# Optimization experiments

Hardware: AMD Instinct MI355X
Metric: run time of the kernel (lower is better)

Reference implementation:

```python
import jax, jax.numpy as jnp
import numpy as np

I4_CLIP = 7.0
NUM_HEADS = 16
NUM_KV_HEADS = 4
HEAD_DIM = 64
ROPE_BASE = 10000.0


def fake_quant_i4(w):
    # per-row int4 symmetric fake quantization with straight-through estimator
    row_max = jnp.maximum(jnp.max(jnp.abs(w), axis=-1, keepdims=True), 1e-8)
    scale = row_max / I4_CLIP
    w_deq = jnp.clip(jnp.round(w / scale), -I4_CLIP, I4_CLIP) * scale
    return w + jax.lax.stop_gradient(w_deq - w)


def rms_norm(x):
    eps = jnp.asarray(jnp.finfo(x.dtype).eps, x.dtype)
    return x * jax.lax.rsqrt(jnp.mean(x * x, axis=-1, keepdims=True) + eps)


def rope_cos_sin(seqlen, dtype):
    inv_freq = 1.0 / (ROPE_BASE ** (jnp.arange(0, HEAD_DIM, 2, dtype=jnp.float32) / HEAD_DIM))
    freqs = jnp.outer(jnp.arange(seqlen, dtype=jnp.float32), inv_freq)  # [S, hd/2]
    return jnp.cos(freqs).astype(dtype), jnp.sin(freqs).astype(dtype)


def apply_rotary(x, cos, sin):
    # x: [B, H, S, hd]; cos/sin: [S, hd/2] broadcast over B, H
    half = x.shape[-1] // 2
    x1, x2 = x[..., :half], x[..., half:]
    return jnp.concatenate((x1 * cos + x2 * sin, -x1 * sin + x2 * cos), axis=-1)


def setup_inputs() -> dict:
    key = jax.random.key(0)
    ks = jax.random.split(key, 6)
    dim = NUM_HEADS * HEAD_DIM
    kv_dim = NUM_KV_HEADS * HEAD_DIM
    return {
        "x": jax.random.normal(ks[0], (2, 2048, dim), jnp.float32),
        "w_q": jax.random.normal(ks[1], (dim, dim), jnp.float32) * 0.02,
        "w_k": jax.random.normal(ks[2], (kv_dim, dim), jnp.float32) * 0.02,
        "w_v": jax.random.normal(ks[3], (kv_dim, dim), jnp.float32) * 0.02,
        "w_proj": jax.random.normal(ks[4], (dim, dim), jnp.float32) * 0.02,
        "q_gain": jnp.ones((NUM_HEADS,), jnp.float32),
    }


def reference(x, w_q, w_k, w_v, w_proj, q_gain):
    bsz, seqlen, dim = x.shape
    rep = NUM_HEADS // NUM_KV_HEADS

    wq, wk, wv, wp = (fake_quant_i4(w) for w in (w_q, w_k, w_v, w_proj))

    # projections: F.linear(x, W) = x @ W.T -> [B, S, out]; split heads -> [B, H, S, hd]
    q = (x @ wq.T).reshape(bsz, seqlen, NUM_HEADS, HEAD_DIM).transpose(0, 2, 1, 3)
    k = (x @ wk.T).reshape(bsz, seqlen, NUM_KV_HEADS, HEAD_DIM).transpose(0, 2, 1, 3)
    v = (x @ wv.T).reshape(bsz, seqlen, NUM_KV_HEADS, HEAD_DIM).transpose(0, 2, 1, 3)

    q, k = rms_norm(q), rms_norm(k)
    cos, sin = rope_cos_sin(seqlen, q.dtype)
    q = apply_rotary(q, cos, sin)
    k = apply_rotary(k, cos, sin)
    q = q * q_gain.astype(q.dtype)[None, :, None, None]

    # GQA: expand kv heads
    k = jnp.repeat(k, rep, axis=1)
    v = jnp.repeat(v, rep, axis=1)

    # causal SDPA
    scale = 1.0 / np.sqrt(HEAD_DIM)
    scores = jnp.einsum("bhqd,bhkd->bhqk", q, k) * scale
    causal = jnp.tril(jnp.ones((seqlen, seqlen), dtype=bool))
    scores = jnp.where(causal, scores, jnp.asarray(-jnp.inf, scores.dtype))
    attn = jax.nn.softmax(scores, axis=-1)
    y = jnp.einsum("bhqk,bhkd->bhqd", attn, v)

    y = y.transpose(0, 2, 1, 3).reshape(bsz, seqlen, dim)
    return y @ wp.T
```

## Files before the change

### kernel.cpp

```cpp
#include <hip/hip_runtime.h>


typedef __bf16 bf16x8 __attribute__((ext_vector_type(8)));
typedef __bf16 bf16x4 __attribute__((ext_vector_type(4)));
typedef float  f32x4  __attribute__((ext_vector_type(4)));

__device__ __forceinline__ unsigned short f2bf(float f) {
  __bf16 h = (__bf16)f;
  return __builtin_bit_cast(unsigned short, h);
}

__global__ void quant_all(const float* __restrict__ wq, const float* __restrict__ wk,
                          const float* __restrict__ wv, const float* __restrict__ wp,
                          unsigned short* __restrict__ wqkv,
                          unsigned short* __restrict__ wpb) {
  int row = blockIdx.x;
  const float* s;
  unsigned short* d;
  if (row < 1024)      { s = wq + (size_t)row * 1024;          d = wqkv + (size_t)row * 1024; }
  else if (row < 1280) { s = wk + (size_t)(row - 1024) * 1024; d = wqkv + (size_t)row * 1024; }
  else if (row < 1536) { s = wv + (size_t)(row - 1280) * 1024; d = wqkv + (size_t)row * 1024; }
  else                 { s = wp + (size_t)(row - 1536) * 1024; d = wpb + (size_t)(row - 1536) * 1024; }
  int t = threadIdx.x;
  float v[4]; float mx = 0.f;
#pragma unroll
  for (int i = 0; i < 4; i++) { v[i] = s[t + 256 * i]; mx = fmaxf(mx, fabsf(v[i])); }
#pragma unroll
  for (int m = 1; m < 64; m <<= 1) mx = fmaxf(mx, __shfl_xor(mx, m));
  __shared__ float smx[4];
  if ((t & 63) == 0) smx[t >> 6] = mx;
  __syncthreads();
  mx = fmaxf(fmaxf(smx[0], smx[1]), fmaxf(smx[2], smx[3]));
  mx = fmaxf(mx, 1e-8f);
  float scale = mx / 7.0f;
#pragma unroll
  for (int i = 0; i < 4; i++) {
    float q = rintf(v[i] / scale);
    q = fminf(fmaxf(q, -7.0f), 7.0f);
    d[t + 256 * i] = f2bf(q * scale);
  }
}

__global__ void cvt_bf16(const float* __restrict__ src,
                         unsigned short* __restrict__ dst, int n) {
  int i = (blockIdx.x * 256 + threadIdx.x) * 4;
  if (i >= n) return;
  float4 f = *(const float4*)(src + i);
  ushort4 o;
  o.x = f2bf(f.x); o.y = f2bf(f.y); o.z = f2bf(f.z); o.w = f2bf(f.w);
  *(ushort4*)(dst + i) = o;
}

#define GLDS(g, l)                                                            \
  __builtin_amdgcn_global_load_lds((const __attribute__((address_space(1))) void*)(g), \
                                   (__attribute__((address_space(3))) void*)(l), 16, 0, 0)

__global__ __launch_bounds__(256, 2) void gemm_bt(
    const unsigned short* __restrict__ A, const unsigned short* __restrict__ Bw,
    float* __restrict__ C, int N, int K, int nbn) {
  int bm = blockIdx.x / nbn, bn = blockIdx.x % nbn;
  int tid = threadIdx.x, w = tid >> 6, lane = tid & 63;
  int l15 = lane & 15, lh = lane >> 4;
  __shared__ __align__(16) unsigned short ldsA[2][128 * 64];
  __shared__ __align__(16) unsigned short ldsB[2][128 * 64];
  int wr = w >> 1, wc = w & 1;
  f32x4 zero = {0.f, 0.f, 0.f, 0.f};
  f32x4 acc[4][4];
#pragma unroll
  for (int i = 0; i < 4; i++)
#pragma unroll
    for (int j = 0; j < 4; j++) acc[i][j] = zero;

  int srow = lane >> 3, schunk = (lane & 7) ^ (lane >> 3);
  const unsigned short* gA0 = A  + (size_t)(bm * 128 + srow) * K + schunk * 8;
  const unsigned short* gB0 = Bw + (size_t)(bn * 128 + srow) * K + schunk * 8;

  int nk = K >> 6;
#pragma unroll
  for (int it = 0; it < 4; it++) {
    int seg = w * 4 + it;
    GLDS(gA0 + (size_t)(seg * 8) * K, (unsigned short*)ldsA[0] + seg * 512);
    GLDS(gB0 + (size_t)(seg * 8) * K, (unsigned short*)ldsB[0] + seg * 512);
  }
  __syncthreads();
  int cur = 0;
  for (int kt = 0; kt < nk; kt++) {
    if (kt + 1 < nk) {
      int k0 = (kt + 1) * 64;
#pragma unroll
      for (int it = 0; it < 4; it++) {
        int seg = w * 4 + it;
        GLDS(gA0 + (size_t)(seg * 8) * K + k0, (unsigned short*)ldsA[cur ^ 1] + seg * 512);
        GLDS(gB0 + (size_t)(seg * 8) * K + k0, (unsigned short*)ldsB[cur ^ 1] + seg * 512);
      }
    }
    const unsigned short* cA = ldsA[cur];
    const unsigned short* cB = ldsB[cur];
#pragma unroll
    for (int ks = 0; ks < 2; ks++) {
      bf16x8 af[4], bfr[4];
#pragma unroll
      for (int fm = 0; fm < 4; fm++) {
        int row = wr * 64 + fm * 16 + l15;
        int slot = (ks * 4 + lh) ^ (row & 7);
        af[fm] = *(const bf16x8*)(cA + row * 64 + slot * 8);
      }
#pragma unroll
      for (int fn = 0; fn < 4; fn++) {
        int row = wc * 64 + fn * 16 + l15;
        int slot = (ks * 4 + lh) ^ (row & 7);
        bfr[fn] = *(const bf16x8*)(cB + row * 64 + slot * 8);
      }
#pragma unroll
      for (int fm = 0; fm < 4; fm++)
#pragma unroll
        for (int fn = 0; fn < 4; fn++)
          acc[fm][fn] = __builtin_amdgcn_mfma_f32_16x16x32_bf16(af[fm], bfr[fn], acc[fm][fn], 0, 0, 0);
    }
    __syncthreads();
    cur ^= 1;
  }
#pragma unroll
  for (int fm = 0; fm < 4; fm++) {
    int r0 = bm * 128 + wr * 64 + fm * 16 + lh * 4;
#pragma unroll
    for (int fn = 0; fn < 4; fn++) {
      int c = bn * 128 + wc * 64 + fn * 16 + l15;
#pragma unroll
      for (int reg = 0; reg < 4; reg++)
        C[(size_t)(r0 + reg) * N + c] = acc[fm][fn][reg];
    }
  }
}

__global__ __launch_bounds__(256, 2) void gemm_qkv(
    const unsigned short* __restrict__ A, const unsigned short* __restrict__ Bw,
    const float* __restrict__ gainp,
    unsigned short* __restrict__ qb, unsigned short* __restrict__ kbp,
    unsigned short* __restrict__ vbp) {
  const int K = 1024;
  int bm = blockIdx.x / 12, bn = blockIdx.x % 12;
  int tid = threadIdx.x, w = tid >> 6, lane = tid & 63;
  int l15 = lane & 15, lh = lane >> 4;
  __shared__ __align__(16) unsigned short ldsA[2][128 * 64];
  __shared__ __align__(16) unsigned short ldsB[2][128 * 64];
  int wr = w >> 1, wc = w & 1;
  f32x4 zero = {0.f, 0.f, 0.f, 0.f};
  f32x4 acc[4][4];
#pragma unroll
  for (int i = 0; i < 4; i++)
#pragma unroll
    for (int j = 0; j < 4; j++) acc[i][j] = zero;

  int srow = lane >> 3, schunk = (lane & 7) ^ (lane >> 3);
  const unsigned short* gA0 = A  + (size_t)(bm * 128 + srow) * K + schunk * 8;
  const unsigned short* gB0 = Bw + (size_t)(bn * 128 + srow) * K + schunk * 8;

#pragma unroll
  for (int it = 0; it < 4; it++) {
    int seg = w * 4 + it;
    GLDS(gA0 + (size_t)(seg * 8) * K, (unsigned short*)ldsA[0] + seg * 512);
    GLDS(gB0 + (size_t)(seg * 8) * K, (unsigned short*)ldsB[0] + seg * 512);
  }
  __syncthreads();
  int cur = 0;
  for (int kt = 0; kt < 16; kt++) {
    if (kt + 1 < 16) {
      int k0 = (kt + 1) * 64;
#pragma unroll
      for (int it = 0; it < 4; it++) {
        int seg = w * 4 + it;
        GLDS(gA0 + (size_t)(seg * 8) * K + k0, (unsigned short*)ldsA[cur ^ 1] + seg * 512);
        GLDS(gB0 + (size_t)(seg * 8) * K + k0, (unsigned short*)ldsB[cur ^ 1] + seg * 512);
      }
    }
    const unsigned short* cA = ldsA[cur];
    const unsigned short* cB = ldsB[cur];
#pragma unroll
    for (int ks = 0; ks < 2; ks++) {
      bf16x8 af[4], bfr[4];
#pragma unroll
      for (int fm = 0; fm < 4; fm++) {
        int row = wr * 64 + fm * 16 + l15;
        int slot = (ks * 4 + lh) ^ (row & 7);
        af[fm] = *(const bf16x8*)(cA + row * 64 + slot * 8);
      }
#pragma unroll
      for (int fn = 0; fn < 4; fn++) {
        int row = wc * 64 + fn * 16 + l15;
        int slot = (ks * 4 + lh) ^ (row & 7);
        bfr[fn] = *(const bf16x8*)(cB + row * 64 + slot * 8);
      }
#pragma unroll
      for (int fm = 0; fm < 4; fm++)
#pragma unroll
        for (int fn = 0; fn < 4; fn++)
          acc[fm][fn] = __builtin_amdgcn_mfma_f32_16x16x32_bf16(af[fm], bfr[fn], acc[fm][fn], 0, 0, 0);
    }
    __syncthreads();
    cur ^= 1;
  }

  int hid = bn * 2 + wc;
  int rbase = bm * 128 + wr * 64;
  if (hid >= 20) {
    int vh = hid - 20;
#pragma unroll
    for (int fm = 0; fm < 4; fm++)
#pragma unroll
      for (int reg = 0; reg < 4; reg++) {
        int r = rbase + fm * 16 + lh * 4 + reg;
        int b = r >> 11, s = r & 2047;
        unsigned short* dst = vbp + (((size_t)(b * 4 + vh) * 2048 + s) << 6);
#pragma unroll
        for (int fn = 0; fn < 4; fn++)
          dst[fn * 16 + l15] = f2bf(acc[fm][fn][reg]);
      }
  } else {
    bool isq = hid < 16;
    float gn = isq ? gainp[hid] : 1.0f;
    float invf0 = __expf(-0.28782313662425572f * (float)l15);
    float invf1 = __expf(-0.28782313662425572f * (float)(l15 + 16));
#pragma unroll
    for (int fm = 0; fm < 4; fm++)
#pragma unroll
      for (int reg = 0; reg < 4; reg++) {
        float y0 = acc[fm][0][reg], y1 = acc[fm][1][reg];
        float y2 = acc[fm][2][reg], y3 = acc[fm][3][reg];
        float ss = y0 * y0 + y1 * y1 + y2 * y2 + y3 * y3;
        ss += __shfl_xor(ss, 1); ss += __shfl_xor(ss, 2);
        ss += __shfl_xor(ss, 4); ss += __shfl_xor(ss, 8);
        float rn = rsqrtf(ss * 0.015625f + 1.1920929e-7f);
        y0 *= rn; y1 *= rn; y2 *= rn; y3 *= rn;
        int r = rbase + fm * 16 + lh * 4 + reg;
        int b = r >> 11, s = r & 2047;
        float c0, s0n, c1, s1n;
        __sincosf((float)s * invf0, &s0n, &c0);
        __sincosf((float)s * invf1, &s1n, &c1);
        float o0 = (y0 * c0 + y2 * s0n) * gn;
        float o1 = (y1 * c1 + y3 * s1n) * gn;
        float o2 = (y2 * c0 - y0 * s0n) * gn;
        float o3 = (y3 * c1 - y1 * s1n) * gn;
        unsigned short* dst = isq
          ? qb  + (((size_t)(b * 16 + hid) * 2048 + s) << 6)
          : kbp + (((size_t)(b * 4 + (hid - 16)) * 2048 + s) << 6);
        dst[l15]      = f2bf(o0);
        dst[l15 + 16] = f2bf(o1);
        dst[l15 + 32] = f2bf(o2);
        dst[l15 + 48] = f2bf(o3);
      }
  }
}

__global__ void v_transpose(const unsigned short* __restrict__ vbp,
                            unsigned short* __restrict__ vt) {
  int bid = blockIdx.x;
  int st = bid & 31, bk = bid >> 5;
  __shared__ unsigned short tile[64][72];
  int t = threadIdx.x;
  int sl = t >> 2, d0 = (t & 3) * 16;
  const unsigned short* src = vbp + (((size_t)bk * 2048 + st * 64 + sl) << 6) + d0;
  *(ushort4*)&tile[sl][d0]      = *(const ushort4*)(src);
  *(ushort4*)&tile[sl][d0 + 4]  = *(const ushort4*)(src + 4);
  *(ushort4*)&tile[sl][d0 + 8]  = *(const ushort4*)(src + 8);
  *(ushort4*)&tile[sl][d0 + 12] = *(const ushort4*)(src + 12);
  __syncthreads();
  int d = t >> 2, p0 = (t & 3) * 16;
  unsigned short* dst = vt + ((size_t)bk * 64 + d) * 2048 + st * 64 + p0;
#pragma unroll
  for (int jo = 0; jo < 16; jo += 4) {
    ushort4 a;
#pragma unroll
    for (int j = 0; j < 4; j++) {
      int p = p0 + jo + j;
      int c = ((p & 3) << 4) | (p >> 2);
      ((unsigned short*)&a)[j] = tile[c][d];
    }
    *(ushort4*)(dst + jo) = a;
  }
}

#define PSTR 72

template<bool MASK>
__device__ __forceinline__ void attn_tile(
    int kv0, int q0, int l15, int lh, float M2,
    const unsigned short* ldsK, const unsigned short* ldsV, unsigned short* pw,
    const bf16x8 (&qf)[4][2], float (&lsum)[4][4], f32x4 (&o)[4][4]) {
  const float K2 = 0.18033688011112042f;
  f32x4 zero = {0.f, 0.f, 0.f, 0.f};
  f32x4 sc[4][4];
#pragma unroll
  for (int fm = 0; fm < 4; fm++)
#pragma unroll
    for (int fn = 0; fn < 4; fn++) sc[fm][fn] = zero;
#pragma unroll
  for (int ks = 0; ks < 2; ks++) {
    bf16x8 kf[4];
#pragma unroll
    for (int fn = 0; fn < 4; fn++) {
      int row = fn * 16 + l15;
      int slot = (ks * 4 + lh) ^ (row & 7);
      kf[fn] = *(const bf16x8*)(ldsK + row * 64 + slot * 8);
    }
#pragma unroll
    for (int fm = 0; fm < 4; fm++)
#pragma unroll
      for (int fn = 0; fn < 4; fn++)
        sc[fm][fn] = __builtin_amdgcn_mfma_f32_16x16x32_bf16(qf[fm][ks], kf[fn], sc[fm][fn], 0, 0, 0);
  }
#pragma unroll
  for (int fm = 0; fm < 4; fm++)
#pragma unroll
    for (int r = 0; r < 4; r++) {
      bf16x4 pk;
      float ls = 0.f;
#pragma unroll
      for (int fn = 0; fn < 4; fn++) {
        float s = __builtin_fmaf(sc[fm][fn][r], K2, -M2);
        if (MASK) {
          int col = kv0 + fn * 16 + l15;
          int row = q0 + fm * 16 + lh * 4 + r;
          if (col > row) s = -1e30f;
        }
        float p = __builtin_amdgcn_exp2f(s);
        ls += p;
        pk[fn] = (__bf16)p;
      }
      *(bf16x4*)(pw + (fm * 16 + lh * 4 + r) * PSTR + l15 * 4) = pk;
      lsum[fm][r] += ls;
    }
  asm volatile("s_waitcnt lgkmcnt(0)" ::: "memory");
  __builtin_amdgcn_sched_barrier(0);
#pragma unroll
  for (int ks2 = 0; ks2 < 2; ks2++) {
    bf16x8 vf[4], pf[4];
#pragma unroll
    for (int fn = 0; fn < 4; fn++) {
      int row = fn * 16 + l15;
      int slot = (ks2 * 4 + lh) ^ (row & 7);
      vf[fn] = *(const bf16x8*)(ldsV + row * 64 + slot * 8);
    }
#pragma unroll
    for (int fm = 0; fm < 4; fm++)
      pf[fm] = *(const bf16x8*)(pw + (fm * 16 + l15) * PSTR + ks2 * 32 + lh * 8);
#pragma unroll
    for (int fm = 0; fm < 4; fm++)
#pragma unroll
      for (int fn = 0; fn < 4; fn++)
        o[fm][fn] = __builtin_amdgcn_mfma_f32_16x16x32_bf16(pf[fm], vf[fn], o[fm][fn], 0, 0, 0);
  }
}

__global__ __launch_bounds__(256, 2) void attn_fwd(
    const unsigned short* __restrict__ qbuf, const unsigned short* __restrict__ kb,
    const unsigned short* __restrict__ vtb, const float* __restrict__ gain,
    unsigned short* __restrict__ ob, unsigned short* __restrict__ pO,
    float* __restrict__ pL) {
  int bid = blockIdx.x;
  int cid = 19 - (bid >> 5);
  int bh = bid & 31;
  int b = bh >> 4, h = bh & 15;
  int qb, ch;
  if (cid < 2)       { qb = cid;                 ch = 0; }
  else if (cid < 6)  { qb = 2 + ((cid - 2) >> 1); ch = (cid - 2) & 1; }
  else if (cid < 12) { qb = 4 + (cid - 6) / 3;    ch = (cid - 6) % 3; }
  else               { qb = 6 + ((cid - 12) >> 2); ch = (cid - 12) & 3; }
  int nt = 4 * qb + 4;
  int t0 = ch * 8;
  int t1 = (t0 + 8 < nt) ? t0 + 8 : nt;
  bool direct = (cid < 2);

  int tid = threadIdx.x;
  int w = tid >> 6, lane = tid & 63;
  int l15 = lane & 15, lh = lane >> 4;
  int q0 = qb * 256 + w * 64;
  int kvh = h >> 2;
  const unsigned short* Q  = qbuf + (size_t)(b * 16 + h) * (2048 * 64);
  const unsigned short* Kg = kb   + (size_t)(b * 4 + kvh) * (2048 * 64);
  const unsigned short* Vg = vtb  + (size_t)(b * 4 + kvh) * (64 * 2048);

  __shared__ __align__(16) unsigned short ldsK[2][64 * 64];
  __shared__ __align__(16) unsigned short ldsV[2][64 * 64];
  __shared__ __align__(16) unsigned short plds[4][64 * PSTR];
  unsigned short* pw = plds[w];

  float gn = gain[h];
  float M2 = __builtin_fmaf(fabsf(gn), 1.46f, 0.02f);

  bf16x8 qf[4][2];
#pragma unroll
  for (int fm = 0; fm < 4; fm++)
#pragma unroll
    for (int ks = 0; ks < 2; ks++)
      qf[fm][ks] = *(const bf16x8*)(Q + (q0 + fm * 16 + l15) * 64 + ks * 32 + lh * 8);

  f32x4 zero = {0.f, 0.f, 0.f, 0.f};
  f32x4 o[4][4];
  float lsum[4][4];
#pragma unroll
  for (int fm = 0; fm < 4; fm++)
#pragma unroll
    for (int r = 0; r < 4; r++) { lsum[fm][r] = 0.f; o[fm][r] = zero; }

  int srow = lane >> 3;
  int schunk = (lane & 7) ^ (lane >> 3);
  int full = q0 >> 6;

#pragma unroll
  for (int it = 0; it < 2; it++) {
    int seg = w * 2 + it;
    GLDS(Kg + (size_t)(t0 * 64 + seg * 8 + srow) * 64 + schunk * 8,
         (unsigned short*)ldsK[0] + seg * 512);
    GLDS(Vg + (size_t)(seg * 8 + srow) * 2048 + t0 * 64 + schunk * 8,
         (unsigned short*)ldsV[0] + seg * 512);
  }
  __syncthreads();
  int cur = 0;
  for (int t = t0; t < t1; t++) {
    int kv0 = t * 64;
    if (t + 1 < t1) {
      int kn = kv0 + 64;
#pragma unroll
      for (int it = 0; it < 2; it++) {
        int seg = w * 2 + it;
        GLDS(Kg + (size_t)(kn + seg * 8 + srow) * 64 + schunk * 8,
             (unsigned short*)ldsK[cur ^ 1] + seg * 512);
        GLDS(Vg + (size_t)(seg * 8 + srow) * 2048 + kn + schunk * 8,
             (unsigned short*)ldsV[cur ^ 1] + seg * 512);
      }
    }
    if (t < full)
      attn_tile<false>(kv0, q0, l15, lh, M2, ldsK[cur], ldsV[cur], pw, qf, lsum, o);
    else if (t == full)
      attn_tile<true>(kv0, q0, l15, lh, M2, ldsK[cur], ldsV[cur], pw, qf, lsum, o);
    __syncthreads();
    cur ^= 1;
  }

  if (direct) {
#pragma unroll
    for (int fm = 0; fm < 4; fm++)
#pragma unroll
      for (int r = 0; r < 4; r++) {
        float l = lsum[fm][r];
        l += __shfl_xor(l, 1); l += __shfl_xor(l, 2);
        l += __shfl_xor(l, 4); l += __shfl_xor(l, 8);
        float inv = 1.0f / l;
        int row = q0 + fm * 16 + lh * 4 + r;
#pragma unroll
        for (int fn = 0; fn < 4; fn++)
          ob[(size_t)(b * 2048 + row) * 1024 + h * 64 + fn * 16 + l15] =
              f2bf(o[fm][fn][r] * inv);
      }
  } else {
    int slot = bh * 18 + (cid - 2);
    unsigned short* po = pO + ((size_t)slot << 14);
    float* pl = pL + slot * 256;
#pragma unroll
    for (int fm = 0; fm < 4; fm++)
#pragma unroll
      for (int r = 0; r < 4; r++) {
        float l = lsum[fm][r];
        l += __shfl_xor(l, 1); l += __shfl_xor(l, 2);
        l += __shfl_xor(l, 4); l += __shfl_xor(l, 8);
        int row = w * 64 + fm * 16 + lh * 4 + r;
        if (l15 == 0) pl[row] = l;
        bf16x4 pv;
#pragma unroll
        for (int fn = 0; fn < 4; fn++) pv[fn] = (__bf16)o[fm][fn][r];
        *(bf16x4*)(po + row * 64 + l15 * 4) = pv;
      }
  }
}

__global__ __launch_bounds__(256) void attn_finalize(
    const unsigned short* __restrict__ pO, const float* __restrict__ pL,
    unsigned short* __restrict__ ob) {
  int bid = blockIdx.x;
  int qb = 2 + bid % 6;
  int bh = bid / 6;
  int b = bh >> 4, h = bh & 15;
  const int ncs[6]   = {2, 2, 3, 3, 4, 4};
  const int sbase[6] = {0, 2, 4, 7, 10, 14};
  int nc = ncs[qb - 2];
  int s0 = bh * 18 + sbase[qb - 2];

  int row = threadIdx.x;
  float acc[64];
#pragma unroll
  for (int j = 0; j < 64; j++) acc[j] = 0.f;
  float l = 0.f;
  for (int c = 0; c < nc; c++) {
    const unsigned short* po = pO + (((size_t)(s0 + c)) << 14) + row * 64;
    l += pL[(s0 + c) * 256 + row];
#pragma unroll
    for (int j = 0; j < 8; j++) {
      uint4 u = *(const uint4*)(po + j * 8);
      const unsigned short* us = (const unsigned short*)&u;
#pragma unroll
      for (int e = 0; e < 8; e++) {
        unsigned int bits = (unsigned int)us[e] << 16;
        acc[j * 8 + e] += __builtin_bit_cast(float, bits);
      }
    }
  }
  float inv = 1.0f / l;
  unsigned short* dst = ob + (size_t)(b * 2048 + qb * 256 + row) * 1024 + h * 64;
  unsigned short outv[64];
#pragma unroll
  for (int c = 0; c < 64; c++) {
    int pos = (c & 15) * 4 + (c >> 4);
    outv[c] = f2bf(acc[pos] * inv);
  }
#pragma unroll
  for (int j = 0; j < 8; j++)
    *(uint4*)(dst + j * 8) = *(const uint4*)(outv + j * 8);
}

extern "C" void kernel_launch(void* const* d_in, const int* in_sizes, int n_in,
                              void* d_out, int out_size, void* d_ws, size_t ws_size,
                              hipStream_t stream) {
  const float* x    = (const float*)d_in[0];
  const float* w_q  = (const float*)d_in[1];
  const float* w_k  = (const float*)d_in[2];
  const float* w_v  = (const float*)d_in[3];
  const float* w_p  = (const float*)d_in[4];
  const float* gain = (const float*)d_in[5];
  float* out = (float*)d_out;

  char* ws = (char*)d_ws;
  unsigned short* x_bf  = (unsigned short*)ws;
  unsigned short* wqkv  = (unsigned short*)(ws + (8u << 20));
  unsigned short* wp    = (unsigned short*)(ws + (11u << 20));
  unsigned short* qbuf  = (unsigned short*)(ws + (13u << 20));
  unsigned short* kbuf  = (unsigned short*)(ws + (21u << 20));
  unsigned short* vbuf  = (unsigned short*)(ws + (23u << 20));
  unsigned short* vtbuf = (unsigned short*)(ws + (25u << 20));
  unsigned short* aout  = (unsigned short*)(ws + (27u << 20));
  unsigned short* pO    = (unsigned short*)(ws + (35u << 20));
  float*          pL    = (float*)(ws + (55u << 20));

  quant_all<<<2560, 256, 0, stream>>>(w_q, w_k, w_v, w_p, wqkv, wp);
  cvt_bf16<<<4096, 256, 0, stream>>>(x, x_bf, 4194304);
  gemm_qkv<<<32 * 12, 256, 0, stream>>>(x_bf, wqkv, gain, qbuf, kbuf, vbuf);
  v_transpose<<<256, 256, 0, stream>>>(vbuf, vtbuf);
  attn_fwd<<<640, 256, 0, stream>>>(qbuf, kbuf, vtbuf, gain, aout, pO, pL);
  attn_finalize<<<192, 256, 0, stream>>>(pO, pL, aout);
  gemm_bt<<<32 * 8, 256, 0, stream>>>(aout, wp, out, 1024, 1024, 8);
}
```

Measured before the change: 114.9 us.

## Halve attention query tile to 128 rows and rebalance KV split-chunks

```diff
diff --git a/kernel.cpp b/kernel.cpp
--- a/kernel.cpp
+++ b/kernel.cpp
@@ -286,12 +286,12 @@
 __device__ __forceinline__ void attn_tile(
     int kv0, int q0, int l15, int lh, float M2,
     const unsigned short* ldsK, const unsigned short* ldsV, unsigned short* pw,
-    const bf16x8 (&qf)[4][2], float (&lsum)[4][4], f32x4 (&o)[4][4]) {
+    const bf16x8 (&qf)[2][2], float (&lsum)[2][4], f32x4 (&o)[2][4]) {
   const float K2 = 0.18033688011112042f;
   f32x4 zero = {0.f, 0.f, 0.f, 0.f};
-  f32x4 sc[4][4];
-#pragma unroll
-  for (int fm = 0; fm < 4; fm++)
+  f32x4 sc[2][4];
+#pragma unroll
+  for (int fm = 0; fm < 2; fm++)
 #pragma unroll
     for (int fn = 0; fn < 4; fn++) sc[fm][fn] = zero;
 #pragma unroll
@@ -304,13 +304,13 @@
       kf[fn] = *(const bf16x8*)(ldsK + row * 64 + slot * 8);
     }
 #pragma unroll
-    for (int fm = 0; fm < 4; fm++)
+    for (int fm = 0; fm < 2; fm++)
 #pragma unroll
       for (int fn = 0; fn < 4; fn++)
         sc[fm][fn] = __builtin_amdgcn_mfma_f32_16x16x32_bf16(qf[fm][ks], kf[fn], sc[fm][fn], 0, 0, 0);
   }
 #pragma unroll
-  for (int fm = 0; fm < 4; fm++)
+  for (int fm = 0; fm < 2; fm++)
 #pragma unroll
     for (int r = 0; r < 4; r++) {
       bf16x4 pk;
@@ -334,7 +334,7 @@
   __builtin_amdgcn_sched_barrier(0);
 #pragma unroll
   for (int ks2 = 0; ks2 < 2; ks2++) {
-    bf16x8 vf[4], pf[4];
+    bf16x8 vf[4], pf[2];
 #pragma unroll
     for (int fn = 0; fn < 4; fn++) {
       int row = fn * 16 + l15;
@@ -342,39 +342,43 @@
       vf[fn] = *(const bf16x8*)(ldsV + row * 64 + slot * 8);
     }
 #pragma unroll
-    for (int fm = 0; fm < 4; fm++)
+    for (int fm = 0; fm < 2; fm++)
       pf[fm] = *(const bf16x8*)(pw + (fm * 16 + l15) * PSTR + ks2 * 32 + lh * 8);
 #pragma unroll
-    for (int fm = 0; fm < 4; fm++)
+    for (int fm = 0; fm < 2; fm++)
 #pragma unroll
       for (int fn = 0; fn < 4; fn++)
         o[fm][fn] = __builtin_amdgcn_mfma_f32_16x16x32_bf16(pf[fm], vf[fn], o[fm][fn], 0, 0, 0);
   }
 }
 
-__global__ __launch_bounds__(256, 2) void attn_fwd(
+__global__ __launch_bounds__(256, 3) void attn_fwd(
     const unsigned short* __restrict__ qbuf, const unsigned short* __restrict__ kb,
     const unsigned short* __restrict__ vtb, const float* __restrict__ gain,
     unsigned short* __restrict__ ob, unsigned short* __restrict__ pO,
     float* __restrict__ pL) {
   int bid = blockIdx.x;
-  int cid = 19 - (bid >> 5);
+  int cid = bid >> 5;
   int bh = bid & 31;
   int b = bh >> 4, h = bh & 15;
-  int qb, ch;
-  if (cid < 2)       { qb = cid;                 ch = 0; }
-  else if (cid < 6)  { qb = 2 + ((cid - 2) >> 1); ch = (cid - 2) & 1; }
-  else if (cid < 12) { qb = 4 + (cid - 6) / 3;    ch = (cid - 6) % 3; }
-  else               { qb = 6 + ((cid - 12) >> 2); ch = (cid - 12) & 3; }
-  int nt = 4 * qb + 4;
-  int t0 = ch * 8;
-  int t1 = (t0 + 8 < nt) ? t0 + 8 : nt;
-  bool direct = (cid < 2);
+  int qb = 0, cum = 0;
+  for (int q = 0; q < 16; q++) {
+    int ncq = (2 * q + 5) >> 2;
+    if (cid < cum + ncq) { qb = q; break; }
+    cum += ncq;
+  }
+  int nt = 2 * qb + 2;
+  int nc = (2 * qb + 5) >> 2;
+  int ch = cid - cum;
+  int base = nt / nc, rem = nt % nc;
+  int t0 = ch * base + (ch < rem ? ch : rem);
+  int t1 = t0 + base + (ch < rem ? 1 : 0);
+  bool direct = (nc == 1);
 
   int tid = threadIdx.x;
   int w = tid >> 6, lane = tid & 63;
   int l15 = lane & 15, lh = lane >> 4;
-  int q0 = qb * 256 + w * 64;
+  int q0 = qb * 128 + w * 32;
   int kvh = h >> 2;
   const unsigned short* Q  = qbuf + (size_t)(b * 16 + h) * (2048 * 64);
   const unsigned short* Kg = kb   + (size_t)(b * 4 + kvh) * (2048 * 64);
@@ -382,24 +386,24 @@
 
   __shared__ __align__(16) unsigned short ldsK[2][64 * 64];
   __shared__ __align__(16) unsigned short ldsV[2][64 * 64];
-  __shared__ __align__(16) unsigned short plds[4][64 * PSTR];
+  __shared__ __align__(16) unsigned short plds[4][32 * PSTR];
   unsigned short* pw = plds[w];
 
   float gn = gain[h];
   float M2 = __builtin_fmaf(fabsf(gn), 1.46f, 0.02f);
 
-  bf16x8 qf[4][2];
-#pragma unroll
-  for (int fm = 0; fm < 4; fm++)
+  bf16x8 qf[2][2];
+#pragma unroll
+  for (int fm = 0; fm < 2; fm++)
 #pragma unroll
     for (int ks = 0; ks < 2; ks++)
       qf[fm][ks] = *(const bf16x8*)(Q + (q0 + fm * 16 + l15) * 64 + ks * 32 + lh * 8);
 
   f32x4 zero = {0.f, 0.f, 0.f, 0.f};
-  f32x4 o[4][4];
-  float lsum[4][4];
-#pragma unroll
-  for (int fm = 0; fm < 4; fm++)
+  f32x4 o[2][4];
+  float lsum[2][4];
+#pragma unroll
+  for (int fm = 0; fm < 2; fm++)
 #pragma unroll
     for (int r = 0; r < 4; r++) { lsum[fm][r] = 0.f; o[fm][r] = zero; }
 
@@ -432,7 +436,7 @@
     }
     if (t < full)
       attn_tile<false>(kv0, q0, l15, lh, M2, ldsK[cur], ldsV[cur], pw, qf, lsum, o);
-    else if (t == full)
+    else if (kv0 <= q0 + 31)
       attn_tile<true>(kv0, q0, l15, lh, M2, ldsK[cur], ldsV[cur], pw, qf, lsum, o);
     __syncthreads();
     cur ^= 1;
@@ -440,7 +444,7 @@
 
   if (direct) {
 #pragma unroll
-    for (int fm = 0; fm < 4; fm++)
+    for (int fm = 0; fm < 2; fm++)
 #pragma unroll
       for (int r = 0; r < 4; r++) {
         float l = lsum[fm][r];
@@ -454,17 +458,17 @@
               f2bf(o[fm][fn][r] * inv);
       }
   } else {
-    int slot = bh * 18 + (cid - 2);
-    unsigned short* po = pO + ((size_t)slot << 14);
-    float* pl = pL + slot * 256;
-#pragma unroll
-    for (int fm = 0; fm < 4; fm++)
+    int slot = bh * 70 + (cid - 2);
+    unsigned short* po = pO + ((size_t)slot << 13);
+    float* pl = pL + slot * 128;
+#pragma unroll
+    for (int fm = 0; fm < 2; fm++)
 #pragma unroll
       for (int r = 0; r < 4; r++) {
         float l = lsum[fm][r];
         l += __shfl_xor(l, 1); l += __shfl_xor(l, 2);
         l += __shfl_xor(l, 4); l += __shfl_xor(l, 8);
-        int row = w * 64 + fm * 16 + lh * 4 + r;
+        int row = w * 32 + fm * 16 + lh * 4 + r;
         if (l15 == 0) pl[row] = l;
         bf16x4 pv;
 #pragma unroll
@@ -474,17 +478,20 @@
   }
 }
 
-__global__ __launch_bounds__(256) void attn_finalize(
+__global__ __launch_bounds__(128) void attn_finalize(
     const unsigned short* __restrict__ pO, const float* __restrict__ pL,
     unsigned short* __restrict__ ob) {
   int bid = blockIdx.x;
-  int qb = 2 + bid % 6;
-  int bh = bid / 6;
+  int qb = 2 + bid % 14;
+  int bh = bid / 14;
   int b = bh >> 4, h = bh & 15;
-  const int ncs[6]   = {2, 2, 3, 3, 4, 4};
-  const int sbase[6] = {0, 2, 4, 7, 10, 14};
-  int nc = ncs[qb - 2];
-  int s0 = bh * 18 + sbase[qb - 2];
+  int cum = 0;
+  for (int q = 0; q < 16; q++) {
+    if (q == qb) break;
+    cum += (2 * q + 5) >> 2;
+  }
+  int nc = (2 * qb + 5) >> 2;
+  int s0 = bh * 70 + (cum - 2);
 
   int row = threadIdx.x;
   float acc[64];
@@ -492,8 +499,8 @@
   for (int j = 0; j < 64; j++) acc[j] = 0.f;
   float l = 0.f;
   for (int c = 0; c < nc; c++) {
-    const unsigned short* po = pO + (((size_t)(s0 + c)) << 14) + row * 64;
-    l += pL[(s0 + c) * 256 + row];
+    const unsigned short* po = pO + (((size_t)(s0 + c)) << 13) + row * 64;
+    l += pL[(s0 + c) * 128 + row];
 #pragma unroll
     for (int j = 0; j < 8; j++) {
       uint4 u = *(const uint4*)(po + j * 8);
@@ -506,7 +513,7 @@
     }
   }
   float inv = 1.0f / l;
-  unsigned short* dst = ob + (size_t)(b * 2048 + qb * 256 + row) * 1024 + h * 64;
+  unsigned short* dst = ob + (size_t)(b * 2048 + qb * 128 + row) * 1024 + h * 64;
   unsigned short outv[64];
 #pragma unroll
   for (int c = 0; c < 64; c++) {
@@ -539,13 +546,13 @@
   unsigned short* vtbuf = (unsigned short*)(ws + (25u << 20));
   unsigned short* aout  = (unsigned short*)(ws + (27u << 20));
   unsigned short* pO    = (unsigned short*)(ws + (35u << 20));
-  float*          pL    = (float*)(ws + (55u << 20));
+  float*          pL    = (float*)(ws + (73u << 20));
 
   quant_all<<<2560, 256, 0, stream>>>(w_q, w_k, w_v, w_p, wqkv, wp);
   cvt_bf16<<<4096, 256, 0, stream>>>(x, x_bf, 4194304);
   gemm_qkv<<<32 * 12, 256, 0, stream>>>(x_bf, wqkv, gain, qbuf, kbuf, vbuf);
   v_transpose<<<256, 256, 0, stream>>>(vbuf, vtbuf);
-  attn_fwd<<<640, 256, 0, stream>>>(qbuf, kbuf, vtbuf, gain, aout, pO, pL);
-  attn_finalize<<<192, 256, 0, stream>>>(pO, pL, aout);
+  attn_fwd<<<2304, 256, 0, stream>>>(qbuf, kbuf, vtbuf, gain, aout, pO, pL);
+  attn_finalize<<<448, 128, 0, stream>>>(pO, pL, aout);
   gemm_bt<<<32 * 8, 256, 0, stream>>>(aout, wp, out, 1024, 1024, 8);
 }
```

Measured after the change: 106.9 us. 6.9% less time.
